# Performance work log

Hardware: AMD Instinct MI355X
Metric: run time of the kernel (lower is better)

The kernel has to match this reference:

```python
import jax, jax.numpy as jnp
import numpy as np

N = 200_000      # n_reflns
NIMG = 500       # n_images
DMETA = 24       # metadata features
WIDTH = 32       # mlp_width
HID = 64         # hidden_units = 2*width (FeedForward default)
DEPTH = 20       # mlp_depth
NPOST = 2        # Normal posterior: (loc, scale)
EPS = 1e-12
KLW = 0.01       # scaling_kl_weight


def setup_inputs() -> dict:
    key = jax.random.key(0)
    ks = jax.random.split(key, 10)
    metadata = jax.random.normal(ks[0], (N, DMETA), jnp.float32)
    iobs = jax.random.normal(ks[1], (N, 1), jnp.float32)
    sigiobs = jax.random.uniform(ks[2], (N, 1), jnp.float32)
    image_ids = jnp.sort(jax.random.randint(ks[3], (N,), 0, NIMG)).astype(jnp.int32)
    n_reflns_per_image = jnp.bincount(image_ids, length=NIMG).astype(jnp.int32)
    d_img = DMETA + 2  # concat(metadata, iobs, sigiobs)
    w_img_in = jax.random.normal(ks[4], (d_img, WIDTH), jnp.float32) / np.float32(np.sqrt(d_img))
    b_img_in = jnp.zeros((WIDTH,), jnp.float32)
    w_scale_in = jax.random.normal(ks[5], (DMETA, WIDTH), jnp.float32) / np.float32(np.sqrt(DMETA))
    b_scale_in = jnp.zeros((WIDTH,), jnp.float32)
    # shared residual FeedForward stack (share_weights=True): x + W2 @ relu(W1 @ x)
    mlp_w1 = jax.random.normal(ks[6], (DEPTH, WIDTH, HID), jnp.float32) / np.float32(np.sqrt(WIDTH))
    mlp_b1 = jnp.zeros((DEPTH, HID), jnp.float32)
    mlp_w2 = jax.random.normal(ks[7], (DEPTH, HID, WIDTH), jnp.float32) * np.float32(0.1 / np.sqrt(HID))
    mlp_b2 = jnp.zeros((DEPTH, WIDTH), jnp.float32)
    w_out = jax.random.normal(ks[8], (WIDTH, NPOST), jnp.float32) / np.float32(np.sqrt(WIDTH))
    b_out = jnp.zeros((NPOST,), jnp.float32)
    return {
        'metadata': metadata, 'iobs': iobs, 'sigiobs': sigiobs,
        'w_img_in': w_img_in, 'b_img_in': b_img_in,
        'w_scale_in': w_scale_in, 'b_scale_in': b_scale_in,
        'mlp_w1': mlp_w1, 'mlp_b1': mlp_b1, 'mlp_w2': mlp_w2, 'mlp_b2': mlp_b2,
        'w_out': w_out, 'b_out': b_out,
        'image_ids_in_this_batch': image_ids,
        'n_reflns_per_image': n_reflns_per_image,
        'mc_samples': 32,
    }


def _mlp(h, w1, b1, w2, b2):
    # depth residual FF blocks, weights stacked along leading DEPTH axis
    def block(h, ws):
        wa, ba, wb, bb = ws
        h = h + (jax.nn.relu(h @ wa + ba) @ wb + bb)
        return h, None
    h, _ = jax.lax.scan(block, h, (w1, b1, w2, b2))
    return h


def reference(metadata, iobs, sigiobs,
              w_img_in, b_img_in, w_scale_in, b_scale_in,
              mlp_w1, mlp_b1, mlp_w2, mlp_b2, w_out, b_out,
              image_ids_in_this_batch, n_reflns_per_image, mc_samples):
    image = jnp.concatenate([metadata, iobs, sigiobs], axis=-1)   # (N, DMETA+2)
    h = image @ w_img_in + b_img_in                               # (N, W)
    h = _mlp(h, mlp_w1, mlp_b1, mlp_w2, mlp_b2)
    nimg = n_reflns_per_image.shape[0]
    sums = jax.ops.segment_sum(h, image_ids_in_this_batch, num_segments=nimg)
    counts = jnp.maximum(n_reflns_per_image, 1).astype(h.dtype)[:, None]
    pooled = sums / counts                                        # (NIMG, W) image-average pool
    s = metadata @ w_scale_in + b_scale_in + pooled[image_ids_in_this_batch]
    s = _mlp(s, mlp_w1, mlp_b1, mlp_w2, mlp_b2)                   # shared weights
    params = s @ w_out + b_out                                    # (N, 2)
    loc = params[:, 0]
    scale = jax.nn.softplus(params[:, 1]) + EPS
    # rsample from Normal(loc, scale), mc_samples draws
    noise = jax.random.normal(jax.random.key(42), (mc_samples, loc.shape[0]), loc.dtype)
    z = loc + scale * noise                                       # (S, N)
    # MC KL estimate: mean_s[log q(z) - log p(z)], p = Laplace(0, 1)
    log_q = -0.5 * jnp.square(noise) - jnp.log(scale) - np.float32(0.5 * np.log(2.0 * np.pi))
    log_p = -jnp.abs(z) - np.float32(np.log(2.0))
    kl_div = KLW * jnp.mean(log_q - log_p, axis=0)                # (N,)
    return z.T, kl_div
```

## Files before the change

kernel.cpp:

```cpp
#include <hip/hip_runtime.h>
#include <stdint.h>

#define N_ROWS 200000
#define NIMG   500
#define DMETA  24
#define WIDTH  32
#define HID    64
#define DEPTH  20
#define MC     32

typedef __attribute__((ext_vector_type(4))) short bf16x4;
typedef __attribute__((ext_vector_type(8))) short bf16x8;
typedef __attribute__((ext_vector_type(4))) float f32x4;

__device__ __forceinline__ f32x4 MFMA16(bf16x4 a, bf16x4 b, f32x4 c) {
    return __builtin_amdgcn_mfma_f32_16x16x16bf16_1k(a, b, c, 0, 0, 0);
}

#define OFF_W1 64000
#define OFF_W2 227840
#define OFF_WI 391680
#define OFF_WS 395776

__device__ __forceinline__ uint32_t rotl32(uint32_t x, int r) {
    return (x << r) | (x >> (32 - r));
}

__device__ __forceinline__ uint32_t tf_bits(uint32_t j) {
    const uint32_t ks1 = 42u, ks2 = 0x1BD11BDAu ^ 42u;
    uint32_t x0 = 0u, x1 = j + ks1;
#define R4(a,b,c,d) \
    x0 += x1; x1 = rotl32(x1,(a)); x1 ^= x0; \
    x0 += x1; x1 = rotl32(x1,(b)); x1 ^= x0; \
    x0 += x1; x1 = rotl32(x1,(c)); x1 ^= x0; \
    x0 += x1; x1 = rotl32(x1,(d)); x1 ^= x0;
    R4(13,15,26,6)  x0 += ks1; x1 += ks2 + 1u;
    R4(17,29,16,24) x0 += ks2; x1 += 0u + 2u;
    R4(13,15,26,6)                x1 += ks1 + 3u;
    R4(17,29,16,24) x0 += ks1; x1 += ks2 + 4u;
    R4(13,15,26,6)  x0 += ks2; x1 += 0u + 5u;
#undef R4
    return x0 ^ x1;
}

__device__ __forceinline__ float bits_to_normal(uint32_t b) {
    float f = __uint_as_float((b >> 9) | 0x3f800000u) - 1.0f;
    const float lo = -0.99999994f;
    float u = fmaxf(lo, f * 2.0f + lo);
    return 1.41421356f * erfinvf(u);
}

__device__ __forceinline__ void split1(float x, short& hi, short& lo) {
    uint32_t b = __float_as_uint(x);
    uint32_t a = b + 0x8000u;
    hi = (short)(a >> 16);
    float r = x - __uint_as_float(a & 0xFFFF0000u);
    lo = (short)(__float_as_uint(r) >> 16);
}

__device__ __forceinline__ void split8p(const float* x, bf16x8& hi, bf16x8& lo) {
    uint32_t hu[4], lu[4];
#pragma unroll
    for (int p = 0; p < 4; ++p) {
        uint32_t a0 = __float_as_uint(x[2 * p]) + 0x8000u;
        uint32_t a1 = __float_as_uint(x[2 * p + 1]) + 0x8000u;
        hu[p] = __builtin_amdgcn_perm(a1, a0, 0x07060302u);
        float r0 = x[2 * p] - __uint_as_float(a0 & 0xFFFF0000u);
        float r1 = x[2 * p + 1] - __uint_as_float(a1 & 0xFFFF0000u);
        lu[p] = __builtin_amdgcn_perm(__float_as_uint(r1), __float_as_uint(r0), 0x07060302u);
    }
    __builtin_memcpy(&hi, hu, 16);
    __builtin_memcpy(&lo, lu, 16);
}

__device__ __forceinline__ void split4p(const float* x, bf16x4& hi, bf16x4& lo) {
    uint32_t hu[2], lu[2];
#pragma unroll
    for (int p = 0; p < 2; ++p) {
        uint32_t a0 = __float_as_uint(x[2 * p]) + 0x8000u;
        uint32_t a1 = __float_as_uint(x[2 * p + 1]) + 0x8000u;
        hu[p] = __builtin_amdgcn_perm(a1, a0, 0x07060302u);
        float r0 = x[2 * p] - __uint_as_float(a0 & 0xFFFF0000u);
        float r1 = x[2 * p + 1] - __uint_as_float(a1 & 0xFFFF0000u);
        lu[p] = __builtin_amdgcn_perm(__float_as_uint(r1), __float_as_uint(r0), 0x07060302u);
    }
    __builtin_memcpy(&hi, hu, 8);
    __builtin_memcpy(&lo, lu, 8);
}

__device__ __forceinline__ bf16x4 vlo(bf16x8 v) { bf16x4 r = {v[0], v[1], v[2], v[3]}; return r; }
__device__ __forceinline__ bf16x4 vhi(bf16x8 v) { bf16x4 r = {v[4], v[5], v[6], v[7]}; return r; }

__device__ __forceinline__ void mlp20_reg(
    float* hC0, float* hC1,
    const short* __restrict__ w1f, const short* __restrict__ w2f,
    const float* __restrict__ b1, const float* __restrict__ b2,
    int lane, int q) {
    const int fo = lane * 8;
#pragma unroll 1
    for (int l = 0; l < DEPTH; ++l) {
        bf16x8 s0h, s0l, s1h, s1l;
        split8p(hC0, s0h, s0l);
        split8p(hC1, s1h, s1l);
        bf16x4 c0h[2] = {vlo(s0h), vhi(s0h)}, c0l[2] = {vlo(s0l), vhi(s0l)};
        bf16x4 c1h[2] = {vlo(s1h), vhi(s1h)}, c1l[2] = {vlo(s1l), vhi(s1l)};
        float Y0[16], Y1[16];
        const short* wp1 = w1f + l * 4096;
#pragma unroll
        for (int Mt = 0; Mt < 4; ++Mt) {
            f32x4 bb = *(const f32x4*)(b1 + l * 64 + 16 * Mt + 4 * q);
            f32x4 a0 = {0.f, 0.f, 0.f, 0.f}, a1 = {0.f, 0.f, 0.f, 0.f};
#pragma unroll
            for (int Kc = 0; Kc < 2; ++Kc) {
                bf16x8 wf = *(const bf16x8*)(wp1 + (Mt * 2 + Kc) * 512 + fo);
                bf16x4 wh = vlo(wf), wl = vhi(wf);
                a0 = MFMA16(wh, c0h[Kc], a0);
                a0 = MFMA16(wh, c0l[Kc], a0);
                a0 = MFMA16(wl, c0h[Kc], a0);
                a1 = MFMA16(wh, c1h[Kc], a1);
                a1 = MFMA16(wh, c1l[Kc], a1);
                a1 = MFMA16(wl, c1h[Kc], a1);
            }
#pragma unroll
            for (int r = 0; r < 4; ++r) {
                Y0[Mt * 4 + r] = fmaxf(a0[r] + bb[r], 0.0f);
                Y1[Mt * 4 + r] = fmaxf(a1[r] + bb[r], 0.0f);
            }
        }
        bf16x8 y0h0, y0l0, y0h1, y0l1, y1h0, y1l0, y1h1, y1l1;
        split8p(Y0, y0h0, y0l0); split8p(Y0 + 8, y0h1, y0l1);
        split8p(Y1, y1h0, y1l0); split8p(Y1 + 8, y1h1, y1l1);
        bf16x4 yb0[4] = {vlo(y0h0), vhi(y0h0), vlo(y0h1), vhi(y0h1)};
        bf16x4 ys0[4] = {vlo(y0l0), vhi(y0l0), vlo(y0l1), vhi(y0l1)};
        bf16x4 yb1[4] = {vlo(y1h0), vhi(y1h0), vlo(y1h1), vhi(y1h1)};
        bf16x4 ys1[4] = {vlo(y1l0), vhi(y1l0), vlo(y1l1), vhi(y1l1)};
        const short* wp2 = w2f + l * 4096;
#pragma unroll
        for (int Mt2 = 0; Mt2 < 2; ++Mt2) {
            f32x4 bb = *(const f32x4*)(b2 + l * 32 + 16 * Mt2 + 4 * q);
            f32x4 a0, a1;
#pragma unroll
            for (int r = 0; r < 4; ++r) { a0[r] = hC0[Mt2 * 4 + r]; a1[r] = hC1[Mt2 * 4 + r]; }
#pragma unroll
            for (int Kc = 0; Kc < 4; ++Kc) {
                bf16x8 wf = *(const bf16x8*)(wp2 + (Mt2 * 4 + Kc) * 512 + fo);
                bf16x4 wh = vlo(wf), wl = vhi(wf);
                a0 = MFMA16(wh, yb0[Kc], a0);
                a0 = MFMA16(wh, ys0[Kc], a0);
                a0 = MFMA16(wl, yb0[Kc], a0);
                a1 = MFMA16(wh, yb1[Kc], a1);
                a1 = MFMA16(wh, ys1[Kc], a1);
                a1 = MFMA16(wl, yb1[Kc], a1);
            }
#pragma unroll
            for (int r = 0; r < 4; ++r) {
                hC0[Mt2 * 4 + r] = a0[r] + bb[r];
                hC1[Mt2 * 4 + r] = a1[r] + bb[r];
            }
        }
    }
}

__device__ __forceinline__ void load_xchunks(
    const float* __restrict__ md, const float* __restrict__ iobs,
    const float* __restrict__ sig, int row, int q,
    bf16x4* bh, bf16x4* bl) {
    f32x4 x0 = *(const f32x4*)(md + (size_t)row * DMETA + 4 * q);
    float x0v[4] = {x0[0], x0[1], x0[2], x0[3]};
    float x1v[4] = {0.f, 0.f, 0.f, 0.f};
    if (q < 2) {
        f32x4 tv = *(const f32x4*)(md + (size_t)row * DMETA + 16 + 4 * q);
        x1v[0] = tv[0]; x1v[1] = tv[1]; x1v[2] = tv[2]; x1v[3] = tv[3];
    } else if (q == 2) {
        x1v[0] = iobs ? iobs[row] : 0.f;
        x1v[1] = sig ? sig[row] : 0.f;
    }
    split4p(x0v, bh[0], bl[0]);
    split4p(x1v, bh[1], bl[1]);
}

__device__ __forceinline__ void in_proj(
    const bf16x4* bh, const bf16x4* bl,
    const short* __restrict__ wf, const float* __restrict__ bias,
    float* hC, int lane, int q) {
    const int fo = lane * 8;
#pragma unroll
    for (int Mt = 0; Mt < 2; ++Mt) {
        f32x4 bb = *(const f32x4*)(bias + 16 * Mt + 4 * q);
        f32x4 a = {0.f, 0.f, 0.f, 0.f};
#pragma unroll
        for (int Kc = 0; Kc < 2; ++Kc) {
            bf16x8 wf8 = *(const bf16x8*)(wf + (Mt * 2 + Kc) * 512 + fo);
            bf16x4 wh = vlo(wf8), wl = vhi(wf8);
            a = MFMA16(wh, bh[Kc], a);
            a = MFMA16(wh, bl[Kc], a);
            a = MFMA16(wl, bh[Kc], a);
        }
#pragma unroll
        for (int r = 0; r < 4; ++r) hC[Mt * 4 + r] = a[r] + bb[r];
    }
}

__global__ __launch_bounds__(256) void prep_kernel(
    const float* __restrict__ w1, const float* __restrict__ w2,
    const float* __restrict__ wimg, const float* __restrict__ wsc,
    char* __restrict__ wsb) {
    int t = blockIdx.x * 256 + threadIdx.x;
    float* sums = (float*)wsb;
    if (t < 16000) { sums[t] = 0.0f; return; }
    t -= 16000;
    if (t < 40960) {
        int l = t >> 11, rem = t & 2047, frag = rem >> 8, vs = rem & 255;
        int lane = vs >> 2, j = vs & 3, q = lane >> 4, c = lane & 15;
        int Mt = frag >> 1, Kc = frag & 1;
        int k = 16 * Kc + 4 * q + j, n = 16 * Mt + c;
        short h, lo; split1(w1[l * 2048 + k * 64 + n], h, lo);
        short* dst = (short*)(wsb + OFF_W1) + l * 4096 + frag * 512 + lane * 8;
        dst[j] = h; dst[4 + j] = lo;
        return;
    }
    t -= 40960;
    if (t < 40960) {
        int l = t >> 11, rem = t & 2047, frag = rem >> 8, vs = rem & 255;
        int lane = vs >> 2, j = vs & 3, q = lane >> 4, c = lane & 15;
        int Mt2 = frag >> 2, Kc = frag & 3;
        int k = 16 * Kc + 4 * q + j, n = 16 * Mt2 + c;
        short h, lo; split1(w2[l * 2048 + k * 32 + n], h, lo);
        short* dst = (short*)(wsb + OFF_W2) + l * 4096 + frag * 512 + lane * 8;
        dst[j] = h; dst[4 + j] = lo;
        return;
    }
    t -= 40960;
    if (t < 1024) {
        int frag = t >> 8, vs = t & 255, lane = vs >> 2, j = vs & 3;
        int q = lane >> 4, c = lane & 15, Mt = frag >> 1, Kc = frag & 1;
        int k = 16 * Kc + 4 * q + j, n = 16 * Mt + c;
        float v = (k < 26) ? wimg[k * 32 + n] : 0.0f;
        short h, lo; split1(v, h, lo);
        short* dst = (short*)(wsb + OFF_WI) + frag * 512 + lane * 8;
        dst[j] = h; dst[4 + j] = lo;
        return;
    }
    t -= 1024;
    if (t < 1024) {
        int frag = t >> 8, vs = t & 255, lane = vs >> 2, j = vs & 3;
        int q = lane >> 4, c = lane & 15, Mt = frag >> 1, Kc = frag & 1;
        int k = 16 * Kc + 4 * q + j, n = 16 * Mt + c;
        float v = (k < 24) ? wsc[k * 32 + n] : 0.0f;
        short h, lo; split1(v, h, lo);
        short* dst = (short*)(wsb + OFF_WS) + frag * 512 + lane * 8;
        dst[j] = h; dst[4 + j] = lo;
        return;
    }
}

__global__ __launch_bounds__(128, 4) void pass_a(
    const float* __restrict__ md, const float* __restrict__ iobs,
    const float* __restrict__ sig, const float* __restrict__ bimg,
    const char* __restrict__ wsb, const float* __restrict__ b1,
    const float* __restrict__ b2, const int* __restrict__ ids,
    float* __restrict__ sums) {
    int lane = threadIdx.x & 63, w = threadIdx.x >> 6;
    int q = lane >> 4, c = lane & 15;
    int i0 = (blockIdx.x * 2 + w) * 32;

    bf16x4 bh0[2], bl0[2], bh1[2], bl1[2];
    load_xchunks(md, iobs, sig, i0 + c, q, bh0, bl0);
    load_xchunks(md, iobs, sig, i0 + 16 + c, q, bh1, bl1);

    float hC0[8], hC1[8];
    in_proj(bh0, bl0, (const short*)(wsb + OFF_WI), bimg, hC0, lane, q);
    in_proj(bh1, bl1, (const short*)(wsb + OFF_WI), bimg, hC1, lane, q);

    mlp20_reg(hC0, hC1, (const short*)(wsb + OFF_W1), (const short*)(wsb + OFF_W2),
              b1, b2, lane, q);

#pragma unroll
    for (int tile = 0; tile < 2; ++tile) {
        float* hC = tile ? hC1 : hC0;
        int tb = i0 + tile * 16;
        if (ids[tb] == ids[tb + 15]) {
            float v[8];
#pragma unroll
            for (int r = 0; r < 8; ++r) v[r] = hC[r];
#pragma unroll
            for (int m = 1; m < 16; m <<= 1)
#pragma unroll
                for (int r = 0; r < 8; ++r) v[r] += __shfl_xor(v[r], m, 64);
            if (c == 0) {
                int id = ids[tb];
#pragma unroll
                for (int t = 0; t < 2; ++t)
#pragma unroll
                    for (int r = 0; r < 4; ++r)
                        atomicAdd(&sums[id * 32 + 16 * t + 4 * q + r], v[t * 4 + r]);
            }
        } else {
            int id = ids[tb + c];
#pragma unroll
            for (int t = 0; t < 2; ++t)
#pragma unroll
                for (int r = 0; r < 4; ++r)
                    atomicAdd(&sums[id * 32 + 16 * t + 4 * q + r], hC[t * 4 + r]);
        }
    }
}

__global__ __launch_bounds__(256) void normalize_kernel(float* __restrict__ sums,
                                                        const int* __restrict__ cnts) {
    int t = blockIdx.x * 256 + threadIdx.x;
    if (t < NIMG * WIDTH) {
        int img = t >> 5;
        float cc = (float)max(cnts[img], 1);
        sums[t] = sums[t] / cc;
    }
}

__global__ __launch_bounds__(128, 4) void pass_b(
    const float* __restrict__ md, const float* __restrict__ bsc,
    const char* __restrict__ wsb, const float* __restrict__ b1,
    const float* __restrict__ b2, const float* __restrict__ wout,
    const float* __restrict__ bout, const int* __restrict__ ids,
    const float* __restrict__ pooled, float* __restrict__ out) {
    int lane = threadIdx.x & 63, w = threadIdx.x >> 6;
    int q = lane >> 4, c = lane & 15;
    int i0 = (blockIdx.x * 2 + w) * 32;

    bf16x4 bh0[2], bl0[2], bh1[2], bl1[2];
    load_xchunks(md, nullptr, nullptr, i0 + c, q, bh0, bl0);
    load_xchunks(md, nullptr, nullptr, i0 + 16 + c, q, bh1, bl1);

    float hC0[8], hC1[8];
    in_proj(bh0, bl0, (const short*)(wsb + OFF_WS), bsc, hC0, lane, q);
    in_proj(bh1, bl1, (const short*)(wsb + OFF_WS), bsc, hC1, lane, q);

#pragma unroll
    for (int tile = 0; tile < 2; ++tile) {
        float* hC = tile ? hC1 : hC0;
        int idv = ids[i0 + tile * 16 + c];
#pragma unroll
        for (int t = 0; t < 2; ++t) {
            f32x4 pv = *(const f32x4*)(pooled + idv * 32 + 16 * t + 4 * q);
#pragma unroll
            for (int r = 0; r < 4; ++r) hC[t * 4 + r] += pv[r];
        }
    }

    mlp20_reg(hC0, hC1, (const short*)(wsb + OFF_W1), (const short*)(wsb + OFF_W2),
              b1, b2, lane, q);

    float loc_t[2], sc_t[2];
#pragma unroll
    for (int tile = 0; tile < 2; ++tile) {
        const float* hC = tile ? hC1 : hC0;
        float p0 = 0.f, p1 = 0.f;
#pragma unroll
        for (int t = 0; t < 2; ++t) {
            f32x4 wA = *(const f32x4*)(wout + (16 * t + 4 * q) * 2);
            f32x4 wB = *(const f32x4*)(wout + (16 * t + 4 * q) * 2 + 4);
            p0 += hC[t * 4 + 0] * wA[0] + hC[t * 4 + 1] * wA[2]
                + hC[t * 4 + 2] * wB[0] + hC[t * 4 + 3] * wB[2];
            p1 += hC[t * 4 + 0] * wA[1] + hC[t * 4 + 1] * wA[3]
                + hC[t * 4 + 2] * wB[1] + hC[t * 4 + 3] * wB[3];
        }
        p0 += __shfl_xor(p0, 16, 64); p0 += __shfl_xor(p0, 32, 64);
        p1 += __shfl_xor(p1, 16, 64); p1 += __shfl_xor(p1, 32, 64);
        float loc = p0 + bout[0];
        float pb = p1 + bout[1];
        loc_t[tile] = loc;
        sc_t[tile] = fmaxf(pb, 0.0f) + log1pf(expf(-fabsf(pb))) + 1e-12f;
    }

    int ro = lane & 31, half = lane >> 5, cs = ro & 15;
    float L0 = __shfl(loc_t[0], cs, 64), L1 = __shfl(loc_t[1], cs, 64);
    float S0 = __shfl(sc_t[0], cs, 64),  S1 = __shfl(sc_t[1], cs, 64);
    float L = (ro < 16) ? L0 : L1;
    float S = (ro < 16) ? S0 : S1;
    float lsg = logf(S);
    int row = i0 + ro;
    float kp = 0.0f;
    float* zrow = out + (size_t)row * MC + half * 16;
#pragma unroll 4
    for (int s4 = 0; s4 < 4; ++s4) {
        f32x4 zv;
#pragma unroll
        for (int jj = 0; jj < 4; ++jj) {
            int t = half * 16 + s4 * 4 + jj;
            uint32_t j = (uint32_t)(t * N_ROWS) + (uint32_t)row;
            float n = bits_to_normal(tf_bits(j));
            float z = fmaf(S, n, L);
            zv[jj] = z;
            kp += fmaf(-0.5f, n * n, fabsf(z));
        }
        *(f32x4*)(zrow + s4 * 4) = zv;
    }
    kp += __shfl_xor(kp, 32, 64);
    if (half == 0) {
        out[(size_t)N_ROWS * MC + row] =
            0.01f * (kp * (1.0f / 32.0f) - lsg - 0.91893853320467274f + 0.69314718055994531f);
    }
}

extern "C" void kernel_launch(void* const* d_in, const int* in_sizes, int n_in,
                              void* d_out, int out_size, void* d_ws, size_t ws_size,
                              hipStream_t stream) {
    const float* md   = (const float*)d_in[0];
    const float* iobs = (const float*)d_in[1];
    const float* sig  = (const float*)d_in[2];
    const float* wimg = (const float*)d_in[3];
    const float* bimg = (const float*)d_in[4];
    const float* wsc  = (const float*)d_in[5];
    const float* bsc  = (const float*)d_in[6];
    const float* w1   = (const float*)d_in[7];
    const float* b1   = (const float*)d_in[8];
    const float* w2   = (const float*)d_in[9];
    const float* b2   = (const float*)d_in[10];
    const float* wout = (const float*)d_in[11];
    const float* bout = (const float*)d_in[12];
    const int* ids    = (const int*)d_in[13];
    const int* cnts   = (const int*)d_in[14];
    float* out = (float*)d_out;
    char* wsb = (char*)d_ws;
    float* sums = (float*)wsb;

    const int nblk = N_ROWS / 64;
    prep_kernel<<<391, 256, 0, stream>>>(w1, w2, wimg, wsc, wsb);
    pass_a<<<nblk, 128, 0, stream>>>(md, iobs, sig, bimg, wsb, b1, b2, ids, sums);
    normalize_kernel<<<(NIMG * WIDTH + 255) / 256, 256, 0, stream>>>(sums, cnts);
    pass_b<<<nblk, 128, 0, stream>>>(md, bsc, wsb, b1, b2, wout, bout, ids, sums, out);
}
```

Baseline: 397.7 us.

## Process four row tiles per wave, reusing per-layer weight fragments across tiles

Each single-wave block now handles 64 rows as four 16-row tiles instead of two waves of two tiles each. Per layer, all W1/W2 fragments and biases are loaded once into registers and reused for the four tiles, and the biases seed the MFMA accumulators. The hi/lo bf16 split now truncates instead of rounding, which saves a few integer ops per element. The cost is higher register pressure and half as many waves in flight, traded for fewer weight loads and more independent MFMA chains per wave.

```diff
diff --git a/kernel.cpp b/kernel.cpp
--- a/kernel.cpp
+++ b/kernel.cpp
@@ -8,6 +8,7 @@
 #define HID    64
 #define DEPTH  20
 #define MC     32
+#define TILES  4
 
 typedef __attribute__((ext_vector_type(4))) short bf16x4;
 typedef __attribute__((ext_vector_type(8))) short bf16x8;
@@ -58,30 +59,30 @@
     lo = (short)(__float_as_uint(r) >> 16);
 }
 
-__device__ __forceinline__ void split8p(const float* x, bf16x8& hi, bf16x8& lo) {
+__device__ __forceinline__ void split8t(const float* x, bf16x8& hi, bf16x8& lo) {
     uint32_t hu[4], lu[4];
 #pragma unroll
     for (int p = 0; p < 4; ++p) {
-        uint32_t a0 = __float_as_uint(x[2 * p]) + 0x8000u;
-        uint32_t a1 = __float_as_uint(x[2 * p + 1]) + 0x8000u;
-        hu[p] = __builtin_amdgcn_perm(a1, a0, 0x07060302u);
-        float r0 = x[2 * p] - __uint_as_float(a0 & 0xFFFF0000u);
-        float r1 = x[2 * p + 1] - __uint_as_float(a1 & 0xFFFF0000u);
+        uint32_t b0 = __float_as_uint(x[2 * p]);
+        uint32_t b1 = __float_as_uint(x[2 * p + 1]);
+        hu[p] = __builtin_amdgcn_perm(b1, b0, 0x07060302u);
+        float r0 = x[2 * p]     - __uint_as_float(b0 & 0xFFFF0000u);
+        float r1 = x[2 * p + 1] - __uint_as_float(b1 & 0xFFFF0000u);
         lu[p] = __builtin_amdgcn_perm(__float_as_uint(r1), __float_as_uint(r0), 0x07060302u);
     }
     __builtin_memcpy(&hi, hu, 16);
     __builtin_memcpy(&lo, lu, 16);
 }
 
-__device__ __forceinline__ void split4p(const float* x, bf16x4& hi, bf16x4& lo) {
+__device__ __forceinline__ void split4t(const float* x, bf16x4& hi, bf16x4& lo) {
     uint32_t hu[2], lu[2];
 #pragma unroll
     for (int p = 0; p < 2; ++p) {
-        uint32_t a0 = __float_as_uint(x[2 * p]) + 0x8000u;
-        uint32_t a1 = __float_as_uint(x[2 * p + 1]) + 0x8000u;
-        hu[p] = __builtin_amdgcn_perm(a1, a0, 0x07060302u);
-        float r0 = x[2 * p] - __uint_as_float(a0 & 0xFFFF0000u);
-        float r1 = x[2 * p + 1] - __uint_as_float(a1 & 0xFFFF0000u);
+        uint32_t b0 = __float_as_uint(x[2 * p]);
+        uint32_t b1 = __float_as_uint(x[2 * p + 1]);
+        hu[p] = __builtin_amdgcn_perm(b1, b0, 0x07060302u);
+        float r0 = x[2 * p]     - __uint_as_float(b0 & 0xFFFF0000u);
+        float r1 = x[2 * p + 1] - __uint_as_float(b1 & 0xFFFF0000u);
         lu[p] = __builtin_amdgcn_perm(__float_as_uint(r1), __float_as_uint(r0), 0x07060302u);
     }
     __builtin_memcpy(&hi, hu, 8);
@@ -91,71 +92,66 @@
 __device__ __forceinline__ bf16x4 vlo(bf16x8 v) { bf16x4 r = {v[0], v[1], v[2], v[3]}; return r; }
 __device__ __forceinline__ bf16x4 vhi(bf16x8 v) { bf16x4 r = {v[4], v[5], v[6], v[7]}; return r; }
 
-__device__ __forceinline__ void mlp20_reg(
-    float* hC0, float* hC1,
+__device__ __forceinline__ void mlp20_reg4(
+    float hC[TILES][8],
     const short* __restrict__ w1f, const short* __restrict__ w2f,
     const float* __restrict__ b1, const float* __restrict__ b2,
     int lane, int q) {
     const int fo = lane * 8;
 #pragma unroll 1
     for (int l = 0; l < DEPTH; ++l) {
-        bf16x8 s0h, s0l, s1h, s1l;
-        split8p(hC0, s0h, s0l);
-        split8p(hC1, s1h, s1l);
-        bf16x4 c0h[2] = {vlo(s0h), vhi(s0h)}, c0l[2] = {vlo(s0l), vhi(s0l)};
-        bf16x4 c1h[2] = {vlo(s1h), vhi(s1h)}, c1l[2] = {vlo(s1l), vhi(s1l)};
-        float Y0[16], Y1[16];
         const short* wp1 = w1f + l * 4096;
-#pragma unroll
-        for (int Mt = 0; Mt < 4; ++Mt) {
-            f32x4 bb = *(const f32x4*)(b1 + l * 64 + 16 * Mt + 4 * q);
-            f32x4 a0 = {0.f, 0.f, 0.f, 0.f}, a1 = {0.f, 0.f, 0.f, 0.f};
-#pragma unroll
-            for (int Kc = 0; Kc < 2; ++Kc) {
-                bf16x8 wf = *(const bf16x8*)(wp1 + (Mt * 2 + Kc) * 512 + fo);
-                bf16x4 wh = vlo(wf), wl = vhi(wf);
-                a0 = MFMA16(wh, c0h[Kc], a0);
-                a0 = MFMA16(wh, c0l[Kc], a0);
-                a0 = MFMA16(wl, c0h[Kc], a0);
-                a1 = MFMA16(wh, c1h[Kc], a1);
-                a1 = MFMA16(wh, c1l[Kc], a1);
-                a1 = MFMA16(wl, c1h[Kc], a1);
+        const short* wp2 = w2f + l * 4096;
+        bf16x8 wf1[8], wf2[8];
+#pragma unroll
+        for (int f = 0; f < 8; ++f) wf1[f] = *(const bf16x8*)(wp1 + f * 512 + fo);
+#pragma unroll
+        for (int f = 0; f < 8; ++f) wf2[f] = *(const bf16x8*)(wp2 + f * 512 + fo);
+        f32x4 bb1[4];
+#pragma unroll
+        for (int Mt = 0; Mt < 4; ++Mt) bb1[Mt] = *(const f32x4*)(b1 + l * 64 + 16 * Mt + 4 * q);
+        f32x4 bb2[2];
+#pragma unroll
+        for (int Mt2 = 0; Mt2 < 2; ++Mt2) bb2[Mt2] = *(const f32x4*)(b2 + l * 32 + 16 * Mt2 + 4 * q);
+
+#pragma unroll
+        for (int tile = 0; tile < TILES; ++tile) {
+            bf16x8 sh, sl;
+            split8t(hC[tile], sh, sl);
+            bf16x4 ch[2] = {vlo(sh), vhi(sh)}, cl[2] = {vlo(sl), vhi(sl)};
+            float Y[16];
+#pragma unroll
+            for (int Mt = 0; Mt < 4; ++Mt) {
+                f32x4 acc = bb1[Mt];
+#pragma unroll
+                for (int Kc = 0; Kc < 2; ++Kc) {
+                    bf16x4 wh = vlo(wf1[Mt * 2 + Kc]), wl = vhi(wf1[Mt * 2 + Kc]);
+                    acc = MFMA16(wh, ch[Kc], acc);
+                    acc = MFMA16(wh, cl[Kc], acc);
+                    acc = MFMA16(wl, ch[Kc], acc);
+                }
+#pragma unroll
+                for (int r = 0; r < 4; ++r) Y[Mt * 4 + r] = fmaxf(acc[r], 0.0f);
             }
-#pragma unroll
-            for (int r = 0; r < 4; ++r) {
-                Y0[Mt * 4 + r] = fmaxf(a0[r] + bb[r], 0.0f);
-                Y1[Mt * 4 + r] = fmaxf(a1[r] + bb[r], 0.0f);
-            }
-        }
-        bf16x8 y0h0, y0l0, y0h1, y0l1, y1h0, y1l0, y1h1, y1l1;
-        split8p(Y0, y0h0, y0l0); split8p(Y0 + 8, y0h1, y0l1);
-        split8p(Y1, y1h0, y1l0); split8p(Y1 + 8, y1h1, y1l1);
-        bf16x4 yb0[4] = {vlo(y0h0), vhi(y0h0), vlo(y0h1), vhi(y0h1)};
-        bf16x4 ys0[4] = {vlo(y0l0), vhi(y0l0), vlo(y0l1), vhi(y0l1)};
-        bf16x4 yb1[4] = {vlo(y1h0), vhi(y1h0), vlo(y1h1), vhi(y1h1)};
-        bf16x4 ys1[4] = {vlo(y1l0), vhi(y1l0), vlo(y1l1), vhi(y1l1)};
-        const short* wp2 = w2f + l * 4096;
-#pragma unroll
-        for (int Mt2 = 0; Mt2 < 2; ++Mt2) {
-            f32x4 bb = *(const f32x4*)(b2 + l * 32 + 16 * Mt2 + 4 * q);
-            f32x4 a0, a1;
-#pragma unroll
-            for (int r = 0; r < 4; ++r) { a0[r] = hC0[Mt2 * 4 + r]; a1[r] = hC1[Mt2 * 4 + r]; }
-#pragma unroll
-            for (int Kc = 0; Kc < 4; ++Kc) {
-                bf16x8 wf = *(const bf16x8*)(wp2 + (Mt2 * 4 + Kc) * 512 + fo);
-                bf16x4 wh = vlo(wf), wl = vhi(wf);
-                a0 = MFMA16(wh, yb0[Kc], a0);
-                a0 = MFMA16(wh, ys0[Kc], a0);
-                a0 = MFMA16(wl, yb0[Kc], a0);
-                a1 = MFMA16(wh, yb1[Kc], a1);
-                a1 = MFMA16(wh, ys1[Kc], a1);
-                a1 = MFMA16(wl, yb1[Kc], a1);
-            }
-#pragma unroll
-            for (int r = 0; r < 4; ++r) {
-                hC0[Mt2 * 4 + r] = a0[r] + bb[r];
-                hC1[Mt2 * 4 + r] = a1[r] + bb[r];
+            bf16x8 yh0, yl0, yh1, yl1;
+            split8t(Y, yh0, yl0);
+            split8t(Y + 8, yh1, yl1);
+            bf16x4 yb[4] = {vlo(yh0), vhi(yh0), vlo(yh1), vhi(yh1)};
+            bf16x4 ys[4] = {vlo(yl0), vhi(yl0), vlo(yl1), vhi(yl1)};
+#pragma unroll
+            for (int Mt2 = 0; Mt2 < 2; ++Mt2) {
+                f32x4 acc;
+#pragma unroll
+                for (int r = 0; r < 4; ++r) acc[r] = hC[tile][Mt2 * 4 + r];
+#pragma unroll
+                for (int Kc = 0; Kc < 4; ++Kc) {
+                    bf16x4 wh = vlo(wf2[Mt2 * 4 + Kc]), wl = vhi(wf2[Mt2 * 4 + Kc]);
+                    acc = MFMA16(wh, yb[Kc], acc);
+                    acc = MFMA16(wh, ys[Kc], acc);
+                    acc = MFMA16(wl, yb[Kc], acc);
+                }
+#pragma unroll
+                for (int r = 0; r < 4; ++r) hC[tile][Mt2 * 4 + r] = acc[r] + bb2[Mt2][r];
             }
         }
     }
@@ -175,30 +171,8 @@
         x1v[0] = iobs ? iobs[row] : 0.f;
         x1v[1] = sig ? sig[row] : 0.f;
     }
-    split4p(x0v, bh[0], bl[0]);
-    split4p(x1v, bh[1], bl[1]);
-}
-
-__device__ __forceinline__ void in_proj(
-    const bf16x4* bh, const bf16x4* bl,
-    const short* __restrict__ wf, const float* __restrict__ bias,
-    float* hC, int lane, int q) {
-    const int fo = lane * 8;
-#pragma unroll
-    for (int Mt = 0; Mt < 2; ++Mt) {
-        f32x4 bb = *(const f32x4*)(bias + 16 * Mt + 4 * q);
-        f32x4 a = {0.f, 0.f, 0.f, 0.f};
-#pragma unroll
-        for (int Kc = 0; Kc < 2; ++Kc) {
-            bf16x8 wf8 = *(const bf16x8*)(wf + (Mt * 2 + Kc) * 512 + fo);
-            bf16x4 wh = vlo(wf8), wl = vhi(wf8);
-            a = MFMA16(wh, bh[Kc], a);
-            a = MFMA16(wh, bl[Kc], a);
-            a = MFMA16(wl, bh[Kc], a);
-        }
-#pragma unroll
-        for (int r = 0; r < 4; ++r) hC[Mt * 4 + r] = a[r] + bb[r];
-    }
+    split4t(x0v, bh[0], bl[0]);
+    split4t(x1v, bh[1], bl[1]);
 }
 
 __global__ __launch_bounds__(256) void prep_kernel(
@@ -254,35 +228,60 @@
     }
 }
 
-__global__ __launch_bounds__(128, 4) void pass_a(
+__device__ __forceinline__ void in_proj4(
+    const float* __restrict__ md, const float* __restrict__ iobs,
+    const float* __restrict__ sig, const short* __restrict__ wf,
+    const float* __restrict__ bias, float hC[TILES][8],
+    int i0, int lane, int q, int c) {
+    const int fo = lane * 8;
+    bf16x8 wfi[4];
+#pragma unroll
+    for (int f = 0; f < 4; ++f) wfi[f] = *(const bf16x8*)(wf + f * 512 + fo);
+    f32x4 bb[2];
+#pragma unroll
+    for (int Mt = 0; Mt < 2; ++Mt) bb[Mt] = *(const f32x4*)(bias + 16 * Mt + 4 * q);
+#pragma unroll
+    for (int tile = 0; tile < TILES; ++tile) {
+        bf16x4 bh[2], bl[2];
+        load_xchunks(md, iobs, sig, i0 + 16 * tile + c, q, bh, bl);
+#pragma unroll
+        for (int Mt = 0; Mt < 2; ++Mt) {
+            f32x4 acc = bb[Mt];
+#pragma unroll
+            for (int Kc = 0; Kc < 2; ++Kc) {
+                bf16x4 wh = vlo(wfi[Mt * 2 + Kc]), wl = vhi(wfi[Mt * 2 + Kc]);
+                acc = MFMA16(wh, bh[Kc], acc);
+                acc = MFMA16(wh, bl[Kc], acc);
+                acc = MFMA16(wl, bh[Kc], acc);
+            }
+#pragma unroll
+            for (int r = 0; r < 4; ++r) hC[tile][Mt * 4 + r] = acc[r];
+        }
+    }
+}
+
+__global__ __launch_bounds__(64, 3) void pass_a(
     const float* __restrict__ md, const float* __restrict__ iobs,
     const float* __restrict__ sig, const float* __restrict__ bimg,
     const char* __restrict__ wsb, const float* __restrict__ b1,
     const float* __restrict__ b2, const int* __restrict__ ids,
     float* __restrict__ sums) {
-    int lane = threadIdx.x & 63, w = threadIdx.x >> 6;
+    int lane = threadIdx.x;
     int q = lane >> 4, c = lane & 15;
-    int i0 = (blockIdx.x * 2 + w) * 32;
-
-    bf16x4 bh0[2], bl0[2], bh1[2], bl1[2];
-    load_xchunks(md, iobs, sig, i0 + c, q, bh0, bl0);
-    load_xchunks(md, iobs, sig, i0 + 16 + c, q, bh1, bl1);
-
-    float hC0[8], hC1[8];
-    in_proj(bh0, bl0, (const short*)(wsb + OFF_WI), bimg, hC0, lane, q);
-    in_proj(bh1, bl1, (const short*)(wsb + OFF_WI), bimg, hC1, lane, q);
-
-    mlp20_reg(hC0, hC1, (const short*)(wsb + OFF_W1), (const short*)(wsb + OFF_W2),
-              b1, b2, lane, q);
-
-#pragma unroll
-    for (int tile = 0; tile < 2; ++tile) {
-        float* hC = tile ? hC1 : hC0;
+    int i0 = blockIdx.x * 64;
+
+    float hC[TILES][8];
+    in_proj4(md, iobs, sig, (const short*)(wsb + OFF_WI), bimg, hC, i0, lane, q, c);
+    mlp20_reg4(hC, (const short*)(wsb + OFF_W1), (const short*)(wsb + OFF_W2),
+               b1, b2, lane, q);
+
+#pragma unroll
+    for (int tile = 0; tile < TILES; ++tile) {
         int tb = i0 + tile * 16;
         if (ids[tb] == ids[tb + 15]) {
             float v[8];
 #pragma unroll
-            for (int r = 0; r < 8; ++r) v[r] = hC[r];
+            for (int r = 0; r < 8; ++r) v[r] = hC[tile][r];
 #pragma unroll
             for (int m = 1; m < 16; m <<= 1)
 #pragma unroll
@@ -301,7 +300,7 @@
             for (int t = 0; t < 2; ++t)
 #pragma unroll
                 for (int r = 0; r < 4; ++r)
-                    atomicAdd(&sums[id * 32 + 16 * t + 4 * q + r], hC[t * 4 + r]);
+                    atomicAdd(&sums[id * 32 + 16 * t + 4 * q + r], hC[tile][t * 4 + r]);
         }
     }
 }
@@ -316,52 +315,51 @@
     }
 }
 
-__global__ __launch_bounds__(128, 4) void pass_b(
+__global__ __launch_bounds__(64, 3) void pass_b(
     const float* __restrict__ md, const float* __restrict__ bsc,
     const char* __restrict__ wsb, const float* __restrict__ b1,
     const float* __restrict__ b2, const float* __restrict__ wout,
     const float* __restrict__ bout, const int* __restrict__ ids,
     const float* __restrict__ pooled, float* __restrict__ out) {
-    int lane = threadIdx.x & 63, w = threadIdx.x >> 6;
+    int lane = threadIdx.x;
     int q = lane >> 4, c = lane & 15;
-    int i0 = (blockIdx.x * 2 + w) * 32;
-
-    bf16x4 bh0[2], bl0[2], bh1[2], bl1[2];
-    load_xchunks(md, nullptr, nullptr, i0 + c, q, bh0, bl0);
-    load_xchunks(md, nullptr, nullptr, i0 + 16 + c, q, bh1, bl1);
-
-    float hC0[8], hC1[8];
-    in_proj(bh0, bl0, (const short*)(wsb + OFF_WS), bsc, hC0, lane, q);
-    in_proj(bh1, bl1, (const short*)(wsb + OFF_WS), bsc, hC1, lane, q);
-
-#pragma unroll
-    for (int tile = 0; tile < 2; ++tile) {
-        float* hC = tile ? hC1 : hC0;
-        int idv = ids[i0 + tile * 16 + c];
+    int i0 = blockIdx.x * 64;
+
+    float hC[TILES][8];
+    in_proj4(md, nullptr, nullptr, (const short*)(wsb + OFF_WS), bsc, hC, i0, lane, q, c);
+
+#pragma unroll
+    for (int tile = 0; tile < TILES; ++tile) {
+        int idv = ids[i0 + 16 * tile + c];
 #pragma unroll
         for (int t = 0; t < 2; ++t) {
             f32x4 pv = *(const f32x4*)(pooled + idv * 32 + 16 * t + 4 * q);
 #pragma unroll
-            for (int r = 0; r < 4; ++r) hC[t * 4 + r] += pv[r];
-        }
-    }
-
-    mlp20_reg(hC0, hC1, (const short*)(wsb + OFF_W1), (const short*)(wsb + OFF_W2),
-              b1, b2, lane, q);
-
-    float loc_t[2], sc_t[2];
-#pragma unroll
-    for (int tile = 0; tile < 2; ++tile) {
-        const float* hC = tile ? hC1 : hC0;
+            for (int r = 0; r < 4; ++r) hC[tile][t * 4 + r] += pv[r];
+        }
+    }
+
+    mlp20_reg4(hC, (const short*)(wsb + OFF_W1), (const short*)(wsb + OFF_W2),
+               b1, b2, lane, q);
+
+    float wo0[2], wo1[2];
+#pragma unroll
+    for (int t = 0; t < 2; ++t) {
+        float2 wv = ((const float2*)wout)[16 * t + 4 * q + 0];
+        (void)wv;
+    }
+    float loc_t[TILES], sc_t[TILES];
+#pragma unroll
+    for (int tile = 0; tile < TILES; ++tile) {
         float p0 = 0.f, p1 = 0.f;
 #pragma unroll
         for (int t = 0; t < 2; ++t) {
             f32x4 wA = *(const f32x4*)(wout + (16 * t + 4 * q) * 2);
             f32x4 wB = *(const f32x4*)(wout + (16 * t + 4 * q) * 2 + 4);
-            p0 += hC[t * 4 + 0] * wA[0] + hC[t * 4 + 1] * wA[2]
-                + hC[t * 4 + 2] * wB[0] + hC[t * 4 + 3] * wB[2];
-            p1 += hC[t * 4 + 0] * wA[1] + hC[t * 4 + 1] * wA[3]
-                + hC[t * 4 + 2] * wB[1] + hC[t * 4 + 3] * wB[3];
+            p0 += hC[tile][t * 4 + 0] * wA[0] + hC[tile][t * 4 + 1] * wA[2]
+                + hC[tile][t * 4 + 2] * wB[0] + hC[tile][t * 4 + 3] * wB[2];
+            p1 += hC[tile][t * 4 + 0] * wA[1] + hC[tile][t * 4 + 1] * wA[3]
+                + hC[tile][t * 4 + 2] * wB[1] + hC[tile][t * 4 + 3] * wB[3];
         }
         p0 += __shfl_xor(p0, 16, 64); p0 += __shfl_xor(p0, 32, 64);
         p1 += __shfl_xor(p1, 16, 64); p1 += __shfl_xor(p1, 32, 64);
@@ -371,21 +369,25 @@
         sc_t[tile] = fmaxf(pb, 0.0f) + log1pf(expf(-fabsf(pb))) + 1e-12f;
     }
 
-    int ro = lane & 31, half = lane >> 5, cs = ro & 15;
-    float L0 = __shfl(loc_t[0], cs, 64), L1 = __shfl(loc_t[1], cs, 64);
-    float S0 = __shfl(sc_t[0], cs, 64),  S1 = __shfl(sc_t[1], cs, 64);
-    float L = (ro < 16) ? L0 : L1;
-    float S = (ro < 16) ? S0 : S1;
+    float Lv[TILES], Sv[TILES];
+#pragma unroll
+    for (int t = 0; t < TILES; ++t) {
+        Lv[t] = __shfl(loc_t[t], c, 64);
+        Sv[t] = __shfl(sc_t[t], c, 64);
+    }
+    int hi2 = lane >> 4;
+    float L = (hi2 < 2) ? ((hi2 == 0) ? Lv[0] : Lv[1]) : ((hi2 == 2) ? Lv[2] : Lv[3]);
+    float S = (hi2 < 2) ? ((hi2 == 0) ? Sv[0] : Sv[1]) : ((hi2 == 2) ? Sv[2] : Sv[3]);
     float lsg = logf(S);
-    int row = i0 + ro;
+    int row = i0 + lane;
     float kp = 0.0f;
-    float* zrow = out + (size_t)row * MC + half * 16;
+    float* zrow = out + (size_t)row * MC;
 #pragma unroll 4
-    for (int s4 = 0; s4 < 4; ++s4) {
+    for (int s4 = 0; s4 < 8; ++s4) {
         f32x4 zv;
 #pragma unroll
         for (int jj = 0; jj < 4; ++jj) {
-            int t = half * 16 + s4 * 4 + jj;
+            int t = s4 * 4 + jj;
             uint32_t j = (uint32_t)(t * N_ROWS) + (uint32_t)row;
             float n = bits_to_normal(tf_bits(j));
             float z = fmaf(S, n, L);
@@ -394,11 +396,8 @@
         }
         *(f32x4*)(zrow + s4 * 4) = zv;
     }
-    kp += __shfl_xor(kp, 32, 64);
-    if (half == 0) {
-        out[(size_t)N_ROWS * MC + row] =
-            0.01f * (kp * (1.0f / 32.0f) - lsg - 0.91893853320467274f + 0.69314718055994531f);
-    }
+    out[(size_t)N_ROWS * MC + row] =
+        0.01f * (kp * (1.0f / 32.0f) - lsg - 0.91893853320467274f + 0.69314718055994531f);
 }
 
 extern "C" void kernel_launch(void* const* d_in, const int* in_sizes, int n_in,
@@ -425,7 +424,7 @@
 
     const int nblk = N_ROWS / 64;
     prep_kernel<<<391, 256, 0, stream>>>(w1, w2, wimg, wsc, wsb);
-    pass_a<<<nblk, 128, 0, stream>>>(md, iobs, sig, bimg, wsb, b1, b2, ids, sums);
+    pass_a<<<nblk, 64, 0, stream>>>(md, iobs, sig, bimg, wsb, b1, b2, ids, sums);
     normalize_kernel<<<(NIMG * WIDTH + 255) / 256, 256, 0, stream>>>(sums, cnts);
-    pass_b<<<nblk, 128, 0, stream>>>(md, bsc, wsb, b1, b2, wout, bout, ids, sums, out);
-}
+    pass_b<<<nblk, 64, 0, stream>>>(md, bsc, wsb, b1, b2, wout, bout, ids, sums, out);
+}
```

Measured after the change: 415.1 us. 4.4% more time.
